# Optimization experiments

Hardware: AMD Instinct MI355X
Metric: run time of the kernel (lower is better)

Reference implementation:

```python
import jax, jax.numpy as jnp
import numpy as np

ALPHA = 0.25
GAMMA = 2.0
W_CLASS = W_BBOX = W_GIOU = W_MASK = W_DICE = W_PROJ = 1.0
EPS = 1e-8


def box_cxcywh_to_xyxy(b):
    cx, cy, w, h = jnp.split(b, 4, axis=-1)
    return jnp.concatenate([cx - 0.5 * w, cy - 0.5 * h, cx + 0.5 * w, cy + 0.5 * h], axis=-1)


def dice_coef(inputs, targets):
    # inputs: logits [N, D]; targets: binary [M, D]
    s = jax.nn.sigmoid(inputs)
    num = 2.0 * jnp.einsum('nd,md->nm', s, targets)
    den = s.sum(-1)[:, None] + targets.sum(-1)[None, :]
    return (num + 1.0) / (den + 1.0)  # [N, M]


def sigmoid_focal_coef(inputs, targets):
    # inputs: logits [N, D]; targets: binary [M, D] -> [N, M]
    x = inputs[:, None, :]
    t = targets[None, :, :]
    p = jax.nn.sigmoid(x)
    # BCE-with-logits, numerically stable
    ce = jnp.maximum(x, 0.0) - x * t + jnp.log1p(jnp.exp(-jnp.abs(x)))
    p_t = p * t + (1.0 - p) * (1.0 - t)
    alpha_t = ALPHA * t + (1.0 - ALPHA) * (1.0 - t)
    return (alpha_t * ce * (1.0 - p_t) ** GAMMA).mean(-1)


def giou_cost(src_xyxy, tgt_xyxy):
    # src [nf, nq, 4], tgt [nf, 1, 4] -> cost [nf, nq, 1]
    a1 = (src_xyxy[..., 2] - src_xyxy[..., 0]) * (src_xyxy[..., 3] - src_xyxy[..., 1])
    a2 = (tgt_xyxy[..., 2] - tgt_xyxy[..., 0]) * (tgt_xyxy[..., 3] - tgt_xyxy[..., 1])
    lt = jnp.maximum(src_xyxy[:, :, None, :2], tgt_xyxy[:, None, :, :2])
    rb = jnp.minimum(src_xyxy[:, :, None, 2:], tgt_xyxy[:, None, :, 2:])
    wh = jnp.clip(rb - lt, 0.0)
    inter = wh[..., 0] * wh[..., 1]
    union = a1[:, :, None] + a2[:, None, :] - inter
    iou = inter / union
    ltc = jnp.minimum(src_xyxy[:, :, None, :2], tgt_xyxy[:, None, :, :2])
    rbc = jnp.maximum(src_xyxy[:, :, None, 2:], tgt_xyxy[:, None, :, 2:])
    whc = jnp.clip(rbc - ltc, 0.0)
    areac = whc[..., 0] * whc[..., 1]
    giou = iou - (areac - union) / areac
    return -giou


def cost_matrix_one(logits, boxes, masks, tmask, tbox, tvalid):
    # logits [nf,nq,1], boxes [nf,nq,4], masks [nf,nq,H,W], tmask [nf,H,W], tbox [nf,4], tvalid [nf]
    p = jax.nn.sigmoid(logits[..., 0])  # [nf, nq]
    neg = (1.0 - ALPHA) * p ** GAMMA * (-jnp.log(1.0 - p + EPS))
    pos = ALPHA * (1.0 - p) ** GAMMA * (-jnp.log(p + EPS))
    w = (tvalid != 0).astype(p.dtype)  # valid-frame mask replaces python `continue`
    cost_class = (((pos - neg) * w[:, None]).sum(0) / w.sum())[:, None]  # [nq, 1]

    cost_bbox = jnp.abs(boxes[:, :, None, :] - tbox[:, None, None, :]).sum(-1).mean(0)  # [nq, 1]
    cost_giou = giou_cost(box_cxcywh_to_xyxy(boxes), box_cxcywh_to_xyxy(tbox[:, None, :])).mean(0)

    out_mask = jnp.transpose(masks, (1, 0, 2, 3))  # [nq, nf, H, W]
    nq = out_mask.shape[0]
    flat_src = out_mask.reshape(nq, -1)
    flat_tgt = tmask.reshape(1, -1)
    cost_mask = sigmoid_focal_coef(flat_src, flat_tgt)  # [nq, 1]
    cost_dice = -dice_coef(flat_src, flat_tgt)

    src_y = jnp.max(out_mask, axis=2, keepdims=True).reshape(nq, -1)  # [nq, nf*W]
    src_x = jnp.max(out_mask, axis=3, keepdims=True).reshape(nq, -1)  # [nq, nf*H]
    tgt_y = jnp.max(tmask[None], axis=2, keepdims=True).reshape(1, -1)
    tgt_x = jnp.max(tmask[None], axis=3, keepdims=True).reshape(1, -1)
    cost_proj = -0.5 * (dice_coef(src_y, tgt_y) + dice_coef(src_x, tgt_x))

    C = (W_CLASS * cost_class + W_BBOX * cost_bbox + W_GIOU * cost_giou
         + W_MASK * cost_mask + W_DICE * cost_dice + W_PROJ * cost_proj)
    return C  # [nq, 1]


def setup_inputs() -> dict:
    key = jax.random.key(0)
    k = jax.random.split(key, 6)
    bs, nf, nq, H, W = 2, 8, 300, 96, 96
    pred_logits = jax.random.normal(k[0], (bs, nf, nq, 1), dtype=jnp.float32)
    pred_boxes = jax.random.uniform(k[1], (bs, nf, nq, 4), dtype=jnp.float32)
    pred_masks = jax.random.normal(k[2], (bs, nf, nq, H, W), dtype=jnp.float32)
    target_masks = (jax.random.uniform(k[3], (bs, nf, H, W)) < 0.3).astype(jnp.float32)
    tgt_boxes = jax.random.uniform(k[4], (bs, nf, 4), dtype=jnp.float32)
    tgt_valid = jnp.ones((bs, nf), dtype=jnp.int32)
    valid_pad = jnp.zeros((bs, H, W), dtype=bool)
    return {"pred_logits": pred_logits, "pred_boxes": pred_boxes, "pred_masks": pred_masks,
            "target_masks": target_masks, "tgt_boxes": tgt_boxes, "tgt_valid": tgt_valid,
            "valid_pad": valid_pad}


def reference(pred_logits, pred_boxes, pred_masks, target_masks, tgt_boxes, tgt_valid, valid_pad):
    # zero out predictions over padded regions (masked_fill with valid[:, None, None])
    masks = jnp.where(valid_pad[:, None, None, :, :], 0.0, pred_masks)
    C = jax.vmap(cost_matrix_one)(pred_logits, pred_boxes, masks, target_masks, tgt_boxes, tgt_valid)
    src_ind = jnp.argmin(C, axis=1).astype(jnp.int64)  # [bs, 1]
    tgt_ind = jnp.zeros_like(src_ind)
    return C, src_ind, tgt_ind
```

## Files before the change

### kernel.cpp

```cpp
#include <hip/hip_runtime.h>
#include <math.h>

#define NF 8
#define NQ 300
#define HSZ 96
#define WSZ 96
#define HW 9216
#define DTOT 73728
#define NT 256
#define NBF 16

#define WS_TGTY 0
#define WS_TGTX 1536
#define WS_TSUM 3072
#define WS_YSUM 3088
#define WS_XSUM 3104
#define WS_TBITS 3200
#define WS_PBITS 7808
#define WS_PART  8448

__device__ __forceinline__ float sigmoid_fast(float x) {
    float e = __expf(-fabsf(x));
    float inv = __builtin_amdgcn_rcpf(1.f + e);
    return x >= 0.f ? inv : e * inv;
}

__device__ __forceinline__ float bf16tof(unsigned short u) {
    return __uint_as_float((unsigned)u << 16);
}

__global__ __launch_bounds__(NT)
void targets_kernel(const float* __restrict__ tm, const unsigned char* __restrict__ vpad,
                    float* __restrict__ ws) {
    int bf = blockIdx.x, t = threadIdx.x;
    int lane = t & 63, wv = t >> 6;
    __shared__ float tile[HSZ * 97];
    __shared__ float red[4][4];
    unsigned long long* tb64 = (unsigned long long*)(ws + WS_TBITS) + bf * 144;
    const float* base = tm + (size_t)bf * HW;
    float tsum = 0.f;
    #pragma unroll
    for (int it = 0; it < 36; ++it) {
        int e = it * NT + t;
        float v = base[e];
        tsum += v;
        unsigned long long bt = __ballot(v != 0.f);
        if (lane == 0) tb64[it * 4 + wv] = bt;
        tile[e + e / 96] = v;
    }
    if ((bf & 7) == 0) {
        int b = bf >> 3;
        unsigned long long* pb64 = (unsigned long long*)(ws + WS_PBITS) + b * 144;
        const unsigned char* pp = vpad + (size_t)b * HW;
        #pragma unroll
        for (int it = 0; it < 36; ++it) {
            int e = it * NT + t;
            unsigned long long bt = __ballot(pp[e] != 0);
            if (lane == 0) pb64[it * 4 + wv] = bt;
        }
    }
    __syncthreads();
    float ysum = 0.f, xsum = 0.f;
    if (t < 96) {
        float m = -INFINITY;
        #pragma unroll 8
        for (int h = 0; h < HSZ; ++h) m = fmaxf(m, tile[h * 97 + t]);
        ws[WS_TGTY + bf * 96 + t] = m;
        ysum = m;
    } else if (t < 192) {
        int hh = t - 96;
        float m = -INFINITY;
        #pragma unroll 8
        for (int w = 0; w < WSZ; ++w) m = fmaxf(m, tile[hh * 97 + w]);
        ws[WS_TGTX + bf * 96 + hh] = m;
        xsum = m;
    }
    float v0 = tsum, v1 = ysum, v2 = xsum;
    #pragma unroll
    for (int off = 32; off > 0; off >>= 1) {
        v0 += __shfl_down(v0, off, 64);
        v1 += __shfl_down(v1, off, 64);
        v2 += __shfl_down(v2, off, 64);
    }
    if (lane == 0) { red[wv][0] = v0; red[wv][1] = v1; red[wv][2] = v2; }
    __syncthreads();
    if (t == 0) {
        #pragma unroll
        for (int w = 1; w < 4; ++w) { v0 += red[w][0]; v1 += red[w][1]; v2 += red[w][2]; }
        ws[WS_TSUM + bf] = v0;
        ws[WS_YSUM + bf] = v1;
        ws[WS_XSUM + bf] = v2;
    }
}

__global__ __launch_bounds__(NT, 8)
void partial_kernel(const float* __restrict__ masks, const float* __restrict__ ws,
                    float* __restrict__ part) {
    int blk = blockIdx.x;
    int bf = blk / NQ;
    int q  = blk - bf * NQ;
    int b  = bf >> 3;
    int t  = threadIdx.x;

    __shared__ unsigned short tile[HSZ * 98];
    __shared__ float scratch[384];

    const float4* mrow = (const float4*)(masks + (size_t)(bf * NQ + q) * HW);
    const unsigned* tb = (const unsigned*)(ws + WS_TBITS) + bf * 288;
    const unsigned* pb = (const unsigned*)(ws + WS_PBITS) + b * 288;

    int widx = t >> 3;
    int sh = (t & 7) * 4;

    float4 cur = mrow[t];
    unsigned twc = tb[widx] >> sh;
    unsigned pwc = pb[widx] >> sh;

    float focal = 0.f, dnum = 0.f, dden = 0.f;

    #pragma unroll
    for (int it = 0; it < 9; ++it) {
        float4 nxt = cur;
        unsigned twn = 0u, pwn = 0u;
        if (it < 8) {
            nxt = mrow[(it + 1) * NT + t];
            twn = tb[(it + 1) * 32 + widx] >> sh;
            pwn = pb[(it + 1) * 32 + widx] >> sh;
        }
        int i4 = it * NT + t;
        int h = i4 / 24;
        int c = (i4 - h * 24) * 4;

        float xs[4] = {cur.x, cur.y, cur.z, cur.w};
        if (pwc & 0xFu) {
            #pragma unroll
            for (int j = 0; j < 4; ++j)
                if ((pwc >> j) & 1u) xs[j] = 0.f;
        }
        unsigned us[4];
        #pragma unroll
        for (int j = 0; j < 4; ++j) {
            float x = xs[j];
            float tg = (float)((twc >> j) & 1u);
            float ee = __expf(-fabsf(x));
            float se = 1.f + ee;
            float inv = __builtin_amdgcn_rcpf(se);
            float s = x >= 0.f ? inv : ee * inv;
            float L = __logf(se);
            float ce = fmaxf(x, 0.f) - x * tg + L;
            float omp = s + tg - 2.f * s * tg;
            float at = 0.75f - 0.5f * tg;
            focal = fmaf(at * ce, omp * omp, focal);
            dnum = fmaf(s, tg, dnum);
            dden += s;
            us[j] = __float_as_uint(x) >> 16;
        }
        int ta = h * 98 + c;
        *(unsigned*)&tile[ta]     = us[0] | (us[1] << 16);
        *(unsigned*)&tile[ta + 2] = us[2] | (us[3] << 16);
        cur = nxt; twc = twn; pwc = pwn;
    }
    __syncthreads();

    if (t < 192) {
        int half = t / 96;
        int u = t - half * 96;
        int k0 = half * 48;
        float mc = -INFINITY, mr = -INFINITY;
        #pragma unroll 4
        for (int k = 0; k < 48; ++k) {
            mc = fmaxf(mc, bf16tof(tile[(k0 + k) * 98 + u]));
            mr = fmaxf(mr, bf16tof(tile[u * 98 + (k0 + k)]));
        }
        scratch[half * 96 + u] = mc;
        scratch[192 + half * 96 + u] = mr;
    }
    __syncthreads();

    float pYn = 0.f, pYd = 0.f, pXn = 0.f, pXd = 0.f;
    if (t < 96) {
        float m = fmaxf(scratch[t], scratch[96 + t]);
        float sg = sigmoid_fast(m);
        pYd = sg;
        pYn = sg * ws[WS_TGTY + bf * 96 + t];
    } else if (t < 192) {
        int r = t - 96;
        float m = fmaxf(scratch[192 + r], scratch[288 + r]);
        float sg = sigmoid_fast(m);
        pXd = sg;
        pXn = sg * ws[WS_TGTX + bf * 96 + r];
    }
    __syncthreads();

    float v[7] = {focal, dnum, dden, pYn, pYd, pXn, pXd};
    #pragma unroll
    for (int k = 0; k < 7; ++k)
        #pragma unroll
        for (int off = 32; off > 0; off >>= 1) v[k] += __shfl_down(v[k], off, 64);
    int wv = t >> 6, lane = t & 63;
    if (lane == 0) {
        #pragma unroll
        for (int k = 0; k < 7; ++k) scratch[wv * 8 + k] = v[k];
    }
    __syncthreads();
    if (t == 0) {
        #pragma unroll
        for (int w = 1; w < 4; ++w)
            #pragma unroll
            for (int k = 0; k < 7; ++k) v[k] += scratch[w * 8 + k];
        float4* p = (float4*)(part + (size_t)blk * 8);
        p[0] = make_float4(v[0], v[1], v[2], v[3]);
        p[1] = make_float4(v[4], v[5], v[6], 0.f);
    }
}

__global__ __launch_bounds__(NT)
void final_kernel(const float* __restrict__ logits, const float* __restrict__ boxes,
                  const float* __restrict__ tbox, const int* __restrict__ tvalid,
                  const float* __restrict__ ws, float* __restrict__ out, int write_idx) {
    int b = blockIdx.x, t = threadIdx.x;
    const float* part = ws + WS_PART;

    float best = INFINITY;
    int bi = 0x7fffffff;

    for (int q = t; q < NQ; q += NT) {
        float focal = 0.f, dnum = 0.f, dden = 0.f;
        float pYn = 0.f, pYd = 0.f, pXn = 0.f, pXd = 0.f;
        float tsum = 0.f, ysum = 0.f, xsum = 0.f;
        #pragma unroll
        for (int f = 0; f < NF; ++f) {
            int bf = b * NF + f;
            const float4* p = (const float4*)(part + (size_t)(bf * NQ + q) * 8);
            float4 pa = p[0], pbv = p[1];
            focal += pa.x; dnum += pa.y; dden += pa.z; pYn += pa.w;
            pYd += pbv.x; pXn += pbv.y; pXd += pbv.z;
            tsum += ws[WS_TSUM + bf];
            ysum += ws[WS_YSUM + bf];
            xsum += ws[WS_XSUM + bf];
        }
        float cost_mask = focal / (float)DTOT;
        float cost_dice = -(2.f * dnum + 1.f) / (dden + tsum + 1.f);
        float coefY = (2.f * pYn + 1.f) / (pYd + ysum + 1.f);
        float coefX = (2.f * pXn + 1.f) / (pXd + xsum + 1.f);
        float cost_proj = -0.5f * (coefY + coefX);

        float wsum = 0.f, cls = 0.f, cb = 0.f, cg = 0.f;
        #pragma unroll
        for (int f = 0; f < NF; ++f) {
            float wv = (tvalid[b * NF + f] != 0) ? 1.f : 0.f;
            wsum += wv;
            float lg = logits[(b * NF + f) * NQ + q];
            float p = sigmoid_fast(lg);
            float negc = 0.75f * p * p * (-__logf(1.f - p + 1e-8f));
            float posc = 0.25f * (1.f - p) * (1.f - p) * (-__logf(p + 1e-8f));
            cls += (posc - negc) * wv;

            const float* bx = boxes + (size_t)((b * NF + f) * NQ + q) * 4;
            const float* tbp = tbox + (b * NF + f) * 4;
            float cx = bx[0], cy = bx[1], bw = bx[2], bh = bx[3];
            float tcx = tbp[0], tcy = tbp[1], tbw = tbp[2], tbh = tbp[3];
            cb += fabsf(cx - tcx) + fabsf(cy - tcy) + fabsf(bw - tbw) + fabsf(bh - tbh);
            float sx1 = cx - 0.5f * bw, sy1 = cy - 0.5f * bh;
            float sx2 = cx + 0.5f * bw, sy2 = cy + 0.5f * bh;
            float tx1 = tcx - 0.5f * tbw, ty1 = tcy - 0.5f * tbh;
            float tx2 = tcx + 0.5f * tbw, ty2 = tcy + 0.5f * tbh;
            float a1 = (sx2 - sx1) * (sy2 - sy1), a2 = (tx2 - tx1) * (ty2 - ty1);
            float iw = fmaxf(fminf(sx2, tx2) - fmaxf(sx1, tx1), 0.f);
            float ih = fmaxf(fminf(sy2, ty2) - fmaxf(sy1, ty1), 0.f);
            float inter = iw * ih;
            float uni = a1 + a2 - inter;
            float iou = inter / uni;
            float cw = fmaxf(fmaxf(sx2, tx2) - fminf(sx1, tx1), 0.f);
            float chh = fmaxf(fmaxf(sy2, ty2) - fminf(sy1, ty1), 0.f);
            float areac = cw * chh;
            cg += -(iou - (areac - uni) / areac);
        }
        cls /= wsum;
        float c = cls + 0.125f * cb + 0.125f * cg + cost_mask + cost_dice + cost_proj;
        out[b * NQ + q] = c;
        if (c < best) { best = c; bi = q; }
    }

    #pragma unroll
    for (int off = 32; off > 0; off >>= 1) {
        float ov = __shfl_down(best, off, 64);
        int oi = __shfl_down(bi, off, 64);
        if (ov < best || (ov == best && oi < bi)) { best = ov; bi = oi; }
    }
    __shared__ float rv[4];
    __shared__ int ri[4];
    int wv = t >> 6, lane = t & 63;
    if (lane == 0) { rv[wv] = best; ri[wv] = bi; }
    __syncthreads();
    if (t == 0 && write_idx) {
        #pragma unroll
        for (int w = 1; w < 4; ++w) {
            if (rv[w] < best || (rv[w] == best && ri[w] < bi)) { best = rv[w]; bi = ri[w]; }
        }
        out[2 * NQ + b] = (float)bi;
        out[2 * NQ + 2 + b] = 0.f;
    }
}

extern "C" void kernel_launch(void* const* d_in, const int* in_sizes, int n_in,
                              void* d_out, int out_size, void* d_ws, size_t ws_size,
                              hipStream_t stream) {
    const float* logits = (const float*)d_in[0];
    const float* boxes  = (const float*)d_in[1];
    const float* masks  = (const float*)d_in[2];
    const float* tmask  = (const float*)d_in[3];
    const float* tbox   = (const float*)d_in[4];
    const int*   tvalid = (const int*)d_in[5];
    const unsigned char* vpad = (const unsigned char*)d_in[6];
    float* out = (float*)d_out;
    float* ws  = (float*)d_ws;

    targets_kernel<<<NBF, NT, 0, stream>>>(tmask, vpad, ws);
    partial_kernel<<<NBF * NQ, NT, 0, stream>>>(masks, ws, ws + WS_PART);
    int write_idx = (out_size >= 2 * NQ + 4) ? 1 : 0;
    final_kernel<<<2, NT, 0, stream>>>(logits, boxes, tbox, tvalid, ws, out, write_idx);
}
```

Before: 345.6 us.

## Compute row/column max projections in registers with 192-thread blocks

The partial kernel now uses 192 threads per block so that each thread always covers the same four columns of every row it processes. Column maxima stay in registers and row maxima are written to small shared arrays, replacing the bf16 tile transpose-and-scan in shared memory. This cuts shared-memory traffic and a synchronization, and projections now use full fp32 instead of truncated bf16 values. In exchange there are fewer threads per block and twelve loop iterations per thread instead of nine.

```diff
diff --git a/kernel.cpp b/kernel.cpp
--- a/kernel.cpp
+++ b/kernel.cpp
@@ -8,6 +8,7 @@
 #define HW 9216
 #define DTOT 73728
 #define NT 256
+#define NTP 192
 #define NBF 16
 
 #define WS_TGTY 0
@@ -23,10 +24,6 @@
     float e = __expf(-fabsf(x));
     float inv = __builtin_amdgcn_rcpf(1.f + e);
     return x >= 0.f ? inv : e * inv;
-}
-
-__device__ __forceinline__ float bf16tof(unsigned short u) {
-    return __uint_as_float((unsigned)u << 16);
 }
 
 __global__ __launch_bounds__(NT)
@@ -93,7 +90,7 @@
     }
 }
 
-__global__ __launch_bounds__(NT, 8)
+__global__ __launch_bounds__(NTP, 8)
 void partial_kernel(const float* __restrict__ masks, const float* __restrict__ ws,
                     float* __restrict__ part) {
     int blk = blockIdx.x;
@@ -101,9 +98,12 @@
     int q  = blk - bf * NQ;
     int b  = bf >> 3;
     int t  = threadIdx.x;
-
-    __shared__ unsigned short tile[HSZ * 98];
-    __shared__ float scratch[384];
+    int w4 = t % 24;
+    int g  = t / 24;
+
+    __shared__ float rowp[HSZ * 25];
+    __shared__ float colp[8 * HSZ];
+    __shared__ float red[3][8];
 
     const float4* mrow = (const float4*)(masks + (size_t)(bf * NQ + q) * HW);
     const unsigned* tb = (const unsigned*)(ws + WS_TBITS) + bf * 288;
@@ -117,27 +117,23 @@
     unsigned pwc = pb[widx] >> sh;
 
     float focal = 0.f, dnum = 0.f, dden = 0.f;
-
-    #pragma unroll
-    for (int it = 0; it < 9; ++it) {
+    float cm0 = -INFINITY, cm1 = -INFINITY, cm2 = -INFINITY, cm3 = -INFINITY;
+
+    #pragma unroll
+    for (int k = 0; k < 12; ++k) {
         float4 nxt = cur;
         unsigned twn = 0u, pwn = 0u;
-        if (it < 8) {
-            nxt = mrow[(it + 1) * NT + t];
-            twn = tb[(it + 1) * 32 + widx] >> sh;
-            pwn = pb[(it + 1) * 32 + widx] >> sh;
-        }
-        int i4 = it * NT + t;
-        int h = i4 / 24;
-        int c = (i4 - h * 24) * 4;
-
+        if (k < 11) {
+            nxt = mrow[(k + 1) * NTP + t];
+            twn = tb[(k + 1) * 24 + widx] >> sh;
+            pwn = pb[(k + 1) * 24 + widx] >> sh;
+        }
         float xs[4] = {cur.x, cur.y, cur.z, cur.w};
         if (pwc & 0xFu) {
             #pragma unroll
             for (int j = 0; j < 4; ++j)
                 if ((pwc >> j) & 1u) xs[j] = 0.f;
         }
-        unsigned us[4];
         #pragma unroll
         for (int j = 0; j < 4; ++j) {
             float x = xs[j];
@@ -153,44 +149,33 @@
             focal = fmaf(at * ce, omp * omp, focal);
             dnum = fmaf(s, tg, dnum);
             dden += s;
-            us[j] = __float_as_uint(x) >> 16;
-        }
-        int ta = h * 98 + c;
-        *(unsigned*)&tile[ta]     = us[0] | (us[1] << 16);
-        *(unsigned*)&tile[ta + 2] = us[2] | (us[3] << 16);
+        }
+        cm0 = fmaxf(cm0, xs[0]); cm1 = fmaxf(cm1, xs[1]);
+        cm2 = fmaxf(cm2, xs[2]); cm3 = fmaxf(cm3, xs[3]);
+        float rm = fmaxf(fmaxf(xs[0], xs[1]), fmaxf(xs[2], xs[3]));
+        rowp[(g + 8 * k) * 25 + w4] = rm;
         cur = nxt; twc = twn; pwc = pwn;
     }
-    __syncthreads();
-
-    if (t < 192) {
-        int half = t / 96;
-        int u = t - half * 96;
-        int k0 = half * 48;
-        float mc = -INFINITY, mr = -INFINITY;
-        #pragma unroll 4
-        for (int k = 0; k < 48; ++k) {
-            mc = fmaxf(mc, bf16tof(tile[(k0 + k) * 98 + u]));
-            mr = fmaxf(mr, bf16tof(tile[u * 98 + (k0 + k)]));
-        }
-        scratch[half * 96 + u] = mc;
-        scratch[192 + half * 96 + u] = mr;
-    }
+    ((float4*)colp)[g * 24 + w4] = make_float4(cm0, cm1, cm2, cm3);
     __syncthreads();
 
     float pYn = 0.f, pYd = 0.f, pXn = 0.f, pXd = 0.f;
     if (t < 96) {
-        float m = fmaxf(scratch[t], scratch[96 + t]);
+        float m = colp[t];
+        #pragma unroll
+        for (int gg = 1; gg < 8; ++gg) m = fmaxf(m, colp[gg * 96 + t]);
         float sg = sigmoid_fast(m);
         pYd = sg;
         pYn = sg * ws[WS_TGTY + bf * 96 + t];
-    } else if (t < 192) {
+    } else {
         int r = t - 96;
-        float m = fmaxf(scratch[192 + r], scratch[288 + r]);
+        float m = rowp[r * 25];
+        #pragma unroll
+        for (int w = 1; w < 24; ++w) m = fmaxf(m, rowp[r * 25 + w]);
         float sg = sigmoid_fast(m);
         pXd = sg;
         pXn = sg * ws[WS_TGTX + bf * 96 + r];
     }
-    __syncthreads();
 
     float v[7] = {focal, dnum, dden, pYn, pYd, pXn, pXd};
     #pragma unroll
@@ -200,14 +185,14 @@
     int wv = t >> 6, lane = t & 63;
     if (lane == 0) {
         #pragma unroll
-        for (int k = 0; k < 7; ++k) scratch[wv * 8 + k] = v[k];
+        for (int k = 0; k < 7; ++k) red[wv][k] = v[k];
     }
     __syncthreads();
     if (t == 0) {
         #pragma unroll
-        for (int w = 1; w < 4; ++w)
+        for (int w = 1; w < 3; ++w)
             #pragma unroll
-            for (int k = 0; k < 7; ++k) v[k] += scratch[w * 8 + k];
+            for (int k = 0; k < 7; ++k) v[k] += red[w][k];
         float4* p = (float4*)(part + (size_t)blk * 8);
         p[0] = make_float4(v[0], v[1], v[2], v[3]);
         p[1] = make_float4(v[4], v[5], v[6], 0.f);
@@ -317,7 +302,7 @@
     float* ws  = (float*)d_ws;
 
     targets_kernel<<<NBF, NT, 0, stream>>>(tmask, vpad, ws);
-    partial_kernel<<<NBF * NQ, NT, 0, stream>>>(masks, ws, ws + WS_PART);
+    partial_kernel<<<NBF * NQ, NTP, 0, stream>>>(masks, ws, ws + WS_PART);
     int write_idx = (out_size >= 2 * NQ + 4) ? 1 : 0;
     final_kernel<<<2, NT, 0, stream>>>(logits, boxes, tbox, tvalid, ws, out, write_idx);
 }
```

New measurement: 409.9 us. +18.6%, slower.
